# Kernel optimization log

Measured on AMD Instinct MI355X. Metric: run time of the kernel, lower is better.

The kernel has to match this reference:

```python
import jax, jax.numpy as jnp
import numpy as np

UPDATE_STEPS = 2
EPS = 1e-7


def _collect(attn, source, W, b):
    """_Collection_Unit: relu(Linear(source)) gathered by attention, row-averaged.
    attn: [N_tgt, N_src], source: [N_src, D_in], W: [D_out, D_in], b: [D_out]."""
    fc_out = jax.nn.relu(source @ W.T + b)          # [N_src, D_out]
    collect = attn @ fc_out                          # [N_tgt, D_out]
    denom = jnp.sum(attn, axis=1, keepdims=True) + EPS
    return collect / denom


def setup_inputs() -> dict:
    key = jax.random.key(0)
    ks = jax.random.split(key, 10)
    N_OBJ, N_REL, D = 2048, 16384, 1024
    inp = {
        "obj_feats": jax.random.normal(ks[0], (N_OBJ, D), jnp.float32),
        "rel_feats": jax.random.normal(ks[1], (N_REL, D), jnp.float32),
        "attn_sub": jax.random.uniform(ks[2], (N_OBJ, N_REL), jnp.float32),
        "attn_obj": jax.random.uniform(ks[3], (N_OBJ, N_REL), jnp.float32),
        "attn_self": jax.random.uniform(ks[4], (N_OBJ, N_OBJ), jnp.float32),
    }
    # normal_init(fc, 0, 0.01) per original module
    names = ["rel2obj_sub", "rel2obj_obj", "obj2rel_sub", "obj2rel_obj", "obj2obj"]
    for i, n in enumerate(names):
        inp[f"W_{n}"] = jax.random.normal(ks[5 + i], (D, D), jnp.float32) * 0.01
        inp[f"b_{n}"] = jnp.zeros((D,), jnp.float32)
    return inp


def reference(obj_feats, rel_feats, attn_sub, attn_obj, attn_self,
              W_rel2obj_sub, b_rel2obj_sub, W_rel2obj_obj, b_rel2obj_obj,
              W_obj2rel_sub, b_obj2rel_sub, W_obj2rel_obj, b_obj2rel_obj,
              W_obj2obj, b_obj2obj):
    x_obj, x_rel = obj_feats, rel_feats
    for _ in range(UPDATE_STEPS):
        # collect to objects: from relations (as subject / as object) and from other objects
        src_sub = _collect(attn_sub, x_rel, W_rel2obj_sub, b_rel2obj_sub)   # unit 0
        src_obj = _collect(attn_obj, x_rel, W_rel2obj_obj, b_rel2obj_obj)   # unit 1
        src_self = _collect(attn_self, x_obj, W_obj2obj, b_obj2obj)         # unit 4
        src2obj = (src_sub + src_obj + src_self) / 3.0
        x_obj_new = x_obj + src2obj                                          # _Update_Unit 0
        # collect to relations: from subject / object node features
        src_rel_sub = _collect(attn_sub.T, x_obj, W_obj2rel_sub, b_obj2rel_sub)  # unit 2
        src_rel_obj = _collect(attn_obj.T, x_obj, W_obj2rel_obj, b_obj2rel_obj)  # unit 3
        src2rel = (src_rel_sub + src_rel_obj) / 2.0
        x_rel = x_rel + src2rel                                              # _Update_Unit 1
        x_obj = x_obj_new
    return x_obj, x_rel
```

## Files before the change

kernel.cpp:

```cpp
#include <hip/hip_runtime.h>
#include <hip/hip_bf16.h>

typedef __attribute__((ext_vector_type(4))) float  f32x4;
typedef __attribute__((ext_vector_type(8))) __bf16 bf16x8;
typedef __attribute__((ext_vector_type(4))) int    i32x4;
typedef __attribute__((ext_vector_type(8))) int    i32x8;
typedef __hip_bfloat16 bf16_t;

#define GT 256
#define BM 128
#define BN 128
#define BK 32

#define NOBJ 2048
#define NREL 16384
#define DIM  1024
#define KOBJ 34816
#define KREL 4096

#define AS1Q __attribute__((address_space(1)))
#define AS3Q __attribute__((address_space(3)))

__device__ __forceinline__ void gload_lds16(const void* g, void* l) {
    __builtin_amdgcn_global_load_lds((AS1Q void*)const_cast<void*>(g),
                                     (AS3Q void*)l, 16, 0, 0);
}

#define MFMA_BF16 __builtin_amdgcn_mfma_f32_16x16x32_bf16
#define MFMA_F8(ACC, Af, Bf) \
    ACC = __builtin_amdgcn_mfma_scale_f32_16x16x128_f8f6f4( \
        Af, Bf, ACC, 0, 0, 0, 0x7F7F7F7F, 0, 0x7F7F7F7F)

__device__ __forceinline__ unsigned char fp8_byte(float x) {
    return (unsigned char)(__builtin_amdgcn_cvt_pk_fp8_f32(x, x, 0, false) & 0xFF);
}
__device__ __forceinline__ unsigned pk4_fp8(float a, float b, float c, float d) {
    int v = __builtin_amdgcn_cvt_pk_fp8_f32(a, b, 0, false);
    v = __builtin_amdgcn_cvt_pk_fp8_f32(c, d, v, true);
    return (unsigned)v;
}

__global__ __launch_bounds__(GT)
void gemm_bt_f234(const bf16_t* __restrict__ A, const bf16_t* __restrict__ B,
                  int M, int N, int K, const float* __restrict__ vecM,
                  unsigned char* __restrict__ fcRel8, unsigned char* __restrict__ fcObj8)
{
    __shared__ bf16_t sA[BM * BK];
    __shared__ bf16_t sB[BN * BK];

    const int tid  = threadIdx.x;
    const int lane = tid & 63;
    const int wid  = tid >> 6;
    const int wr = wid >> 1, wc = wid & 1;
    const int l15 = lane & 15, lk = lane >> 4;

    const long rowA0 = (long)blockIdx.x * BM;
    const long rowB0 = (long)blockIdx.y * BN;
    const long ldab  = (long)K * 2;

    const int c0 = tid, c1 = tid + GT;
    const int r0c = c0 >> 2, k0c = (c0 & 3) ^ ((r0c >> 1) & 3);
    const int r1c = c1 >> 2, k1c = (c1 & 3) ^ ((r1c >> 1) & 3);

    const char* gA0 = (const char*)A + (rowA0 + r0c) * ldab + k0c * 16;
    const char* gA1 = (const char*)A + (rowA0 + r1c) * ldab + k1c * 16;
    const char* gB0 = (const char*)B + (rowB0 + r0c) * ldab + k0c * 16;
    const char* gB1 = (const char*)B + (rowB0 + r1c) * ldab + k1c * 16;
    char* lA0 = (char*)sA + c0 * 16;
    char* lA1 = (char*)sA + c1 * 16;
    char* lB0 = (char*)sB + c0 * 16;
    char* lB1 = (char*)sB + c1 * 16;

    f32x4 acc[4][4];
    #pragma unroll
    for (int i = 0; i < 4; i++)
        #pragma unroll
        for (int j = 0; j < 4; j++) acc[i][j] = f32x4{0.f, 0.f, 0.f, 0.f};

    const int ktPer = K / BK;
    for (int kt = 0; kt < ktPer; ++kt) {
        const long kByte = (long)kt * (BK * 2);
        gload_lds16(gA0 + kByte, lA0);
        gload_lds16(gA1 + kByte, lA1);
        gload_lds16(gB0 + kByte, lB0);
        gload_lds16(gB1 + kByte, lB1);
        __syncthreads();

        bf16x8 af[4], bg[4];
        #pragma unroll
        for (int i = 0; i < 4; i++) {
            const int rr = wr * 64 + i * 16 + l15;
            const int kk = lk ^ ((rr >> 1) & 3);
            af[i] = *reinterpret_cast<const bf16x8*>((const char*)sA + rr * 64 + kk * 16);
        }
        #pragma unroll
        for (int j = 0; j < 4; j++) {
            const int rr = wc * 64 + j * 16 + l15;
            const int kk = lk ^ ((rr >> 1) & 3);
            bg[j] = *reinterpret_cast<const bf16x8*>((const char*)sB + rr * 64 + kk * 16);
        }
        #pragma unroll
        for (int i = 0; i < 4; i++)
            #pragma unroll
            for (int j = 0; j < 4; j++)
                acc[i][j] = MFMA_BF16(af[i], bg[j], acc[i][j], 0, 0, 0);
        __syncthreads();
    }

    #pragma unroll
    for (int i = 0; i < 4; i++) {
        const long mBase = rowA0 + wr * 64 + i * 16 + lk * 4;
        const f32x4 vm = *reinterpret_cast<const f32x4*>(&vecM[mBase]);
        #pragma unroll
        for (int r = 0; r < 4; r++) {
            const long m = mBase + r;
            #pragma unroll
            for (int j = 0; j < 4; j++) {
                const long n = rowB0 + wc * 64 + j * 16 + l15;
                const float v = fmaxf(acc[i][j][r] + vm[r], 0.f) * 64.f;
                const unsigned char o = fp8_byte(v);
                if (m < 1024)            fcRel8[m * (long)KREL + n] = o;
                else if (m < 2048)       fcRel8[(m - 1024) * (long)KREL + 2048 + n] = o;
                else                     fcObj8[(m - 2048) * (long)KOBJ + 32768 + n] = o;
            }
        }
    }
}

__global__ __launch_bounds__(512, 4)
void gemmf8fc(const unsigned char* __restrict__ A, const unsigned char* __restrict__ B,
              const float* __restrict__ bias, unsigned char* __restrict__ Cb8)
{
    __shared__ __align__(16) char lds[49152];

    const int tid  = threadIdx.x;
    const int lane = tid & 63;
    const int wid  = tid >> 6;
    const int wr = wid >> 2, wc = wid & 3;
    const int l15 = lane & 15, lk = lane >> 4;

    const int bid = blockIdx.x;
    const int s   = (bid & 7) * 128 + (bid >> 3);
    const long rowM0 = (long)(s >> 6) * 128;
    const long rowN0 = (long)(s & 63) * 256;
    const int  K  = 1024;
    const long ld = (long)K;
    const int  NT = K >> 7;

    const int rs = tid >> 3;
    const int kc = (tid & 7) ^ (rs & 7);
    const char* gA = (const char*)A + (rowM0 + rs) * ld + kc * 16;
    const char* gB = (const char*)B + (rowN0 + rs) * ld + kc * 16;
    char* lA = (char*)lds + tid * 16;
    char* lB = (char*)lds + 16384 + tid * 16;

    const int xc0 = ((2 * lk + 0) ^ (l15 & 7)) * 16;
    const int xc1 = ((2 * lk + 1) ^ (l15 & 7)) * 16;
    const int baseA = (wr * 64 + l15) * 128;
    const int baseB = 16384 + (wc * 64 + l15) * 128;

#define LDF8(dst, off) { \
    i32x4 lo_ = *(const i32x4*)((const char*)lds + (off) + xc0); \
    i32x4 hi_ = *(const i32x4*)((const char*)lds + (off) + xc1); \
    dst = __builtin_shufflevector(lo_, hi_, 0, 1, 2, 3, 4, 5, 6, 7); }

    f32x4 acc[4][4];
    #pragma unroll
    for (int i = 0; i < 4; i++)
        #pragma unroll
        for (int j = 0; j < 4; j++) acc[i][j] = f32x4{0.f, 0.f, 0.f, 0.f};

    for (int t = 0; t < NT; ++t) {
        const long kByte = (long)t * 128;
        gload_lds16(gA + kByte, lA);
        gload_lds16(gA + kByte + 64 * ld, lA + 8192);
        #pragma unroll
        for (int i = 0; i < 4; i++)
            gload_lds16(gB + kByte + (long)i * 64 * ld, lB + i * 8192);
        __syncthreads();

        i32x8 a[4];
        #pragma unroll
        for (int kf = 0; kf < 4; kf++) LDF8(a[kf], baseA + kf * 2048);
        #pragma unroll
        for (int j = 0; j < 4; j++) {
            i32x8 b;
            LDF8(b, baseB + j * 2048);
            #pragma unroll
            for (int kf = 0; kf < 4; kf++) MFMA_F8(acc[kf][j], a[kf], b);
        }
        __syncthreads();
    }
#undef LDF8

    #pragma unroll
    for (int kf = 0; kf < 4; kf++) {
        const long m0 = rowM0 + wr * 64 + kf * 16 + lk * 4;
        #pragma unroll
        for (int r = 0; r < 4; r++) {
            const long m = m0 + r;
            const float bs = 64.f * bias[m];
            #pragma unroll
            for (int j = 0; j < 4; j++) {
                const long n = rowN0 + wc * 64 + j * 16 + l15;
                const float v = fmaxf(acc[kf][j][r] + bs, 0.f);
                Cb8[(m & 1023) * (long)KOBJ + (m >> 10) * 16384 + n] = fp8_byte(v);
            }
        }
    }
}

__global__ __launch_bounds__(512, 4)
void gemmf8_dual(const unsigned char* __restrict__ Ao, const unsigned char* __restrict__ Bo,
                 float* __restrict__ Co,
                 const unsigned char* __restrict__ Ar, const unsigned char* __restrict__ Br,
                 float* __restrict__ Cr)
{
    __shared__ __align__(16) char lds[49152];

    const int tid  = threadIdx.x;
    const int lane = tid & 63;
    const int wid  = tid >> 6;
    const int wr = wid >> 2, wc = wid & 3;
    const int l15 = lane & 15, lk = lane >> 4;

    const int bid = blockIdx.x;
    const int s   = (bid & 7) * 128 + (bid >> 3);

    const unsigned char* A; const unsigned char* B; float* C;
    int K, NT; long kb0; float scale; bool at;
    long rowM0, rowN0;
    if (s < 512) {
        const int zz = s >> 6, t = s & 63;
        rowM0 = (long)(t >> 2) * 128; rowN0 = (long)(t & 3) * 256;
        A = Ao; B = Bo; C = Co;
        K = KOBJ; NT = 34; kb0 = (long)34 * zz * 128;
        scale = 1.f / (8192.f * 64.f); at = true;
    } else {
        const int t = s - 512;
        rowM0 = (long)(t >> 2) * 128; rowN0 = (long)(t & 3) * 256;
        A = Ar; B = Br; C = Cr;
        K = KREL; NT = 32; kb0 = 0;
        scale = 1.f / (2048.f * 64.f); at = false;
    }
    const long ld = (long)K;

    const int rs = tid >> 3;
    const int kc = (tid & 7) ^ (rs & 7);
    const char* gA = (const char*)A + (rowM0 + rs) * ld + kb0 + kc * 16;
    const char* gB = (const char*)B + (rowN0 + rs) * ld + kb0 + kc * 16;
    char* lA = (char*)lds + tid * 16;
    char* lB = (char*)lds + 16384 + tid * 16;

    const int xc0 = ((2 * lk + 0) ^ (l15 & 7)) * 16;
    const int xc1 = ((2 * lk + 1) ^ (l15 & 7)) * 16;
    const int baseA = (wr * 64 + l15) * 128;
    const int baseB = 16384 + (wc * 64 + l15) * 128;

#define LDF8(dst, off) { \
    i32x4 lo_ = *(const i32x4*)((const char*)lds + (off) + xc0); \
    i32x4 hi_ = *(const i32x4*)((const char*)lds + (off) + xc1); \
    dst = __builtin_shufflevector(lo_, hi_, 0, 1, 2, 3, 4, 5, 6, 7); }

    f32x4 acc[4][4];
    #pragma unroll
    for (int i = 0; i < 4; i++)
        #pragma unroll
        for (int j = 0; j < 4; j++) acc[i][j] = f32x4{0.f, 0.f, 0.f, 0.f};

    for (int t = 0; t < NT; ++t) {
        const long kByte = (long)t * 128;
        gload_lds16(gA + kByte, lA);
        gload_lds16(gA + kByte + 64 * ld, lA + 8192);
        #pragma unroll
        for (int i = 0; i < 4; i++)
            gload_lds16(gB + kByte + (long)i * 64 * ld, lB + i * 8192);
        __syncthreads();

        i32x8 a[4];
        #pragma unroll
        for (int kf = 0; kf < 4; kf++) LDF8(a[kf], baseA + kf * 2048);
        #pragma unroll
        for (int j = 0; j < 4; j++) {
            i32x8 b;
            LDF8(b, baseB + j * 2048);
            #pragma unroll
            for (int kf = 0; kf < 4; kf++) MFMA_F8(acc[kf][j], a[kf], b);
        }
        __syncthreads();
    }
#undef LDF8

    #pragma unroll
    for (int kf = 0; kf < 4; kf++) {
        const long m0 = rowM0 + wr * 64 + kf * 16 + lk * 4;
        #pragma unroll
        for (int r = 0; r < 4; r++) {
            const long m = m0 + r;
            #pragma unroll
            for (int j = 0; j < 4; j++) {
                const long n = rowN0 + wc * 64 + j * 16 + l15;
                const float v = acc[kf][j][r] * scale;
                if (at) atomicAdd(&C[m * (long)DIM + n], v);
                else    C[m * (long)DIM + n] += v;
            }
        }
    }
}

__global__ __launch_bounds__(256)
void k_cast_bf16(const float* __restrict__ in, bf16_t* __restrict__ out, long n)
{
    const long stride = (long)gridDim.x * blockDim.x;
    for (long i = (long)blockIdx.x * blockDim.x + threadIdx.x; i * 4 < n; i += stride) {
        f32x4 v = *reinterpret_cast<const f32x4*>(in + i * 4);
        union { bf16_t h[4]; ushort4 u; } o;
        o.h[0] = __float2bfloat16(v[0]); o.h[1] = __float2bfloat16(v[1]);
        o.h[2] = __float2bfloat16(v[2]); o.h[3] = __float2bfloat16(v[3]);
        *reinterpret_cast<ushort4*>(out + i * 4) = o.u;
    }
}

__global__ __launch_bounds__(256)
void k_cast_fp8(const float* __restrict__ in, unsigned char* __restrict__ out,
                long n, float scale)
{
    const long stride = (long)gridDim.x * blockDim.x;
    for (long i = (long)blockIdx.x * blockDim.x + threadIdx.x; i * 4 < n; i += stride) {
        f32x4 v = *reinterpret_cast<const f32x4*>(in + i * 4);
        *reinterpret_cast<unsigned*>(out + i * 4) =
            pk4_fp8(v[0] * scale, v[1] * scale, v[2] * scale, v[3] * scale);
    }
}

template<bool COLS>
__global__ __launch_bounds__(256)
void k_sums(const float* __restrict__ in, int C,
            float* __restrict__ rowsum, float* __restrict__ colsum)
{
    __shared__ float cpart[16][64];
    __shared__ float rpart[64][17];
    const int tid = threadIdx.x;
    const int tx  = tid & 15;
    const int ty  = tid >> 4;
    const long c0 = (long)blockIdx.x * 64;
    const long r0 = (long)blockIdx.y * 64;

    float cs0 = 0.f, cs1 = 0.f, cs2 = 0.f, cs3 = 0.f;
    #pragma unroll
    for (int i = 0; i < 4; i++) {
        const int r = i * 16 + ty;
        const f32x4 v = *reinterpret_cast<const f32x4*>(&in[(r0 + r) * (long)C + c0 + tx * 4]);
        rpart[r][tx] = v[0] + v[1] + v[2] + v[3];
        cs0 += v[0]; cs1 += v[1]; cs2 += v[2]; cs3 += v[3];
    }
    if (COLS) {
        cpart[ty][tx * 4 + 0] = cs0;
        cpart[ty][tx * 4 + 1] = cs1;
        cpart[ty][tx * 4 + 2] = cs2;
        cpart[ty][tx * 4 + 3] = cs3;
    }
    __syncthreads();
    if (tid < 64) {
        float rs = 0.f;
        #pragma unroll
        for (int k = 0; k < 16; k++) rs += rpart[tid][k];
        atomicAdd(&rowsum[r0 + tid], rs);
        if (COLS) {
            float cs = 0.f;
            #pragma unroll
            for (int k = 0; k < 16; k++) cs += cpart[k][tid];
            atomicAdd(&colsum[c0 + tid], cs);
        }
    }
}

__global__ __launch_bounds__(256)
void k_invscale(float* __restrict__ s, int n, float c)
{
    const int i = blockIdx.x * 256 + threadIdx.x;
    if (i < n) s[i] = c / (s[i] + 1e-7f);
}

template<bool TRANS>
__global__ __launch_bounds__(256)
void k_prep2f8(const float* __restrict__ in, int C,
               unsigned char* __restrict__ Aobj, unsigned char* __restrict__ Arel,
               const float* __restrict__ invRow, const float* __restrict__ invCol)
{
    __shared__ float tile[64][65];
    const int tid = threadIdx.x;
    const int tx  = tid & 15;
    const int ty  = tid >> 4;
    const long c0 = (long)blockIdx.x * 64;
    const long r0 = (long)blockIdx.y * 64;

    #pragma unroll
    for (int i = 0; i < 4; i++) {
        const int r = i * 16 + ty;
        const f32x4 v = *reinterpret_cast<const f32x4*>(&in[(r0 + r) * (long)C + c0 + tx * 4]);
        const float sc = invRow[r0 + r];
        *reinterpret_cast<unsigned*>(&Aobj[(r0 + r) * (long)KOBJ + c0 + tx * 4]) =
            pk4_fp8(v[0] * sc, v[1] * sc, v[2] * sc, v[3] * sc);
        if (TRANS) *reinterpret_cast<f32x4*>(&tile[r][tx * 4]) = v;
    }
    if (TRANS) {
        __syncthreads();
        const int rr = tid & 63;
        const int cg = tid >> 6;
        #pragma unroll
        for (int i = 0; i < 16; i++) {
            const int c = cg * 16 + i;
            const float sc = invCol[c0 + c];
            Arel[(c0 + c) * (long)KREL + r0 + rr] = fp8_byte(tile[rr][c] * sc);
        }
    }
}

extern "C" void kernel_launch(void* const* d_in, const int* in_sizes, int n_in,
                              void* d_out, int out_size, void* d_ws, size_t ws_size,
                              hipStream_t stream)
{
    if (n_in < 15) return;
    const float* obj_feats = (const float*)d_in[0];
    const float* rel_feats = (const float*)d_in[1];
    const float* attn_sub  = (const float*)d_in[2];
    const float* attn_obj  = (const float*)d_in[3];
    const float* attn_self = (const float*)d_in[4];
    const float* Wf[5] = { (const float*)d_in[5], (const float*)d_in[7],
                           (const float*)d_in[9], (const float*)d_in[11], (const float*)d_in[13] };
    const float* Bf[5] = { (const float*)d_in[6], (const float*)d_in[8],
                           (const float*)d_in[10], (const float*)d_in[12], (const float*)d_in[14] };

    const int NO = NOBJ, NR = NREL, D = DIM;

    char* w = (char*)d_ws;
    auto take = [&](size_t bytes) { char* p = w; w += bytes; return p; };
    unsigned char* Aobj8  = (unsigned char*)take((size_t)NO * KOBJ);
    unsigned char* Arel8  = (unsigned char*)take((size_t)NR * KREL);
    unsigned char* fcObj8 = (unsigned char*)take((size_t)D * KOBJ);
    unsigned char* fcRel8 = (unsigned char*)take((size_t)D * KREL);
    unsigned char* xrel8  = (unsigned char*)take((size_t)NR * D);
    unsigned char* W018   = (unsigned char*)take((size_t)2 * D * D);
    bf16_t* xobj_bf = (bf16_t*)take((size_t)NO * D * 2);
    bf16_t* Wstk234 = (bf16_t*)take((size_t)3 * D * D * 2);
    float*  b01     = (float*)take((size_t)2 * D * 4);
    float*  bstk    = (float*)take((size_t)3 * D * 4);
    float*  sums    = (float*)take((size_t)(3 * NO + 2 * NR) * 4);
    float* invS     = sums;
    float* invO     = sums + NO;
    float* invSelf  = sums + 2 * NO;
    float* invTS    = sums + 3 * NO;
    float* invTO    = sums + 3 * NO + NR;
    if ((size_t)(w - (char*)d_ws) > ws_size) return;

    float* x_obj = (float*)d_out;
    float* x_rel = x_obj + (size_t)NO * D;

    hipMemcpyAsync(x_obj, obj_feats, (size_t)NO * D * 4, hipMemcpyDeviceToDevice, stream);
    hipMemcpyAsync(x_rel, rel_feats, (size_t)NR * D * 4, hipMemcpyDeviceToDevice, stream);
    hipMemcpyAsync(b01,     Bf[0], (size_t)D * 4, hipMemcpyDeviceToDevice, stream);
    hipMemcpyAsync(b01 + D, Bf[1], (size_t)D * 4, hipMemcpyDeviceToDevice, stream);
    for (int i = 0; i < 3; i++)
        hipMemcpyAsync(bstk + i * D, Bf[2 + i], (size_t)D * 4, hipMemcpyDeviceToDevice, stream);
    hipMemsetAsync(sums, 0, (size_t)(3 * NO + 2 * NR) * 4, stream);

    auto castb = [&](const float* in, bf16_t* out, long n) {
        long blocks = (n / 4 + 255) / 256; if (blocks > 4096) blocks = 4096;
        k_cast_bf16<<<dim3((unsigned)blocks), dim3(256), 0, stream>>>(in, out, n);
    };
    auto cast8 = [&](const float* in, unsigned char* out, long n, float sc) {
        long blocks = (n / 4 + 255) / 256; if (blocks > 4096) blocks = 4096;
        k_cast_fp8<<<dim3((unsigned)blocks), dim3(256), 0, stream>>>(in, out, n, sc);
    };
    cast8(Wf[0], W018,                 (long)D * D, 64.f);
    cast8(Wf[1], W018 + (size_t)D * D, (long)D * D, 64.f);
    for (int i = 0; i < 3; i++)
        castb(Wf[2 + i], Wstk234 + (size_t)i * D * D, (long)D * D);

    k_sums<true><<<dim3(NR / 64, NO / 64), dim3(256), 0, stream>>>(attn_sub, NR, invS, invTS);
    k_sums<true><<<dim3(NR / 64, NO / 64), dim3(256), 0, stream>>>(attn_obj, NR, invO, invTO);
    k_sums<false><<<dim3(NO / 64, NO / 64), dim3(256), 0, stream>>>(attn_self, NO, invSelf, nullptr);
    k_invscale<<<dim3((3 * NO + 255) / 256), dim3(256), 0, stream>>>(sums, 3 * NO, 8192.f / 3.f);
    k_invscale<<<dim3((2 * NR + 255) / 256), dim3(256), 0, stream>>>(sums + 3 * NO, 2 * NR, 1024.f);

    k_prep2f8<true><<<dim3(NR / 64, NO / 64), dim3(256), 0, stream>>>(
        attn_sub, NR, Aobj8, Arel8, invS, invTS);
    k_prep2f8<true><<<dim3(NR / 64, NO / 64), dim3(256), 0, stream>>>(
        attn_obj, NR, Aobj8 + 16384, Arel8 + 2048, invO, invTO);
    k_prep2f8<false><<<dim3(NO / 64, NO / 64), dim3(256), 0, stream>>>(
        attn_self, NO, Aobj8 + 32768, nullptr, invSelf, nullptr);

    for (int step = 0; step < 2; ++step) {
        castb(x_obj, xobj_bf, (long)NO * D);
        cast8(x_rel, xrel8, (long)NR * D, 1.f);

        gemmf8fc<<<dim3(1024), dim3(512), 0, stream>>>(W018, xrel8, b01, fcObj8);
        gemm_bt_f234<<<dim3(3 * D / BM, NO / BN, 1), dim3(GT), 0, stream>>>(
            Wstk234, xobj_bf, 3 * D, NO, D, bstk, fcRel8, fcObj8);

        gemmf8_dual<<<dim3(1024), dim3(512), 0, stream>>>(
            Aobj8, fcObj8, x_obj, Arel8, fcRel8, x_rel);
    }
}
```

Measured before the change: 813.8 us.

## Merge object-side FC GEMMs into FP8 MLP kernel and fuse x_rel FP8 cast into update

Replaces the bf16 GEMM for units 2-4 with FP8 by casting those weights and x_obj to FP8. That GEMM is merged with the relation-side FC GEMM into one launch of 1216 blocks, and a block-index branch picks the operands. The relation update epilogue now also writes the FP8 copy of x_rel, so the separate per-step x_rel cast pass goes away. This cuts kernel launches, memory traffic and matrix-core cost, but lowers the precision of the object-feature MLP to FP8.

```diff
diff --git a/kernel.cpp b/kernel.cpp
--- a/kernel.cpp
+++ b/kernel.cpp
@@ -7,11 +7,6 @@
 typedef __attribute__((ext_vector_type(8))) int    i32x8;
 typedef __hip_bfloat16 bf16_t;
 
-#define GT 256
-#define BM 128
-#define BN 128
-#define BK 32
-
 #define NOBJ 2048
 #define NREL 16384
 #define DIM  1024
@@ -26,7 +21,6 @@
                                      (AS3Q void*)l, 16, 0, 0);
 }
 
-#define MFMA_BF16 __builtin_amdgcn_mfma_f32_16x16x32_bf16
 #define MFMA_F8(ACC, Af, Bf) \
     ACC = __builtin_amdgcn_mfma_scale_f32_16x16x128_f8f6f4( \
         Af, Bf, ACC, 0, 0, 0, 0x7F7F7F7F, 0, 0x7F7F7F7F)
@@ -40,96 +34,11 @@
     return (unsigned)v;
 }
 
-__global__ __launch_bounds__(GT)
-void gemm_bt_f234(const bf16_t* __restrict__ A, const bf16_t* __restrict__ B,
-                  int M, int N, int K, const float* __restrict__ vecM,
-                  unsigned char* __restrict__ fcRel8, unsigned char* __restrict__ fcObj8)
-{
-    __shared__ bf16_t sA[BM * BK];
-    __shared__ bf16_t sB[BN * BK];
-
-    const int tid  = threadIdx.x;
-    const int lane = tid & 63;
-    const int wid  = tid >> 6;
-    const int wr = wid >> 1, wc = wid & 1;
-    const int l15 = lane & 15, lk = lane >> 4;
-
-    const long rowA0 = (long)blockIdx.x * BM;
-    const long rowB0 = (long)blockIdx.y * BN;
-    const long ldab  = (long)K * 2;
-
-    const int c0 = tid, c1 = tid + GT;
-    const int r0c = c0 >> 2, k0c = (c0 & 3) ^ ((r0c >> 1) & 3);
-    const int r1c = c1 >> 2, k1c = (c1 & 3) ^ ((r1c >> 1) & 3);
-
-    const char* gA0 = (const char*)A + (rowA0 + r0c) * ldab + k0c * 16;
-    const char* gA1 = (const char*)A + (rowA0 + r1c) * ldab + k1c * 16;
-    const char* gB0 = (const char*)B + (rowB0 + r0c) * ldab + k0c * 16;
-    const char* gB1 = (const char*)B + (rowB0 + r1c) * ldab + k1c * 16;
-    char* lA0 = (char*)sA + c0 * 16;
-    char* lA1 = (char*)sA + c1 * 16;
-    char* lB0 = (char*)sB + c0 * 16;
-    char* lB1 = (char*)sB + c1 * 16;
-
-    f32x4 acc[4][4];
-    #pragma unroll
-    for (int i = 0; i < 4; i++)
-        #pragma unroll
-        for (int j = 0; j < 4; j++) acc[i][j] = f32x4{0.f, 0.f, 0.f, 0.f};
-
-    const int ktPer = K / BK;
-    for (int kt = 0; kt < ktPer; ++kt) {
-        const long kByte = (long)kt * (BK * 2);
-        gload_lds16(gA0 + kByte, lA0);
-        gload_lds16(gA1 + kByte, lA1);
-        gload_lds16(gB0 + kByte, lB0);
-        gload_lds16(gB1 + kByte, lB1);
-        __syncthreads();
-
-        bf16x8 af[4], bg[4];
-        #pragma unroll
-        for (int i = 0; i < 4; i++) {
-            const int rr = wr * 64 + i * 16 + l15;
-            const int kk = lk ^ ((rr >> 1) & 3);
-            af[i] = *reinterpret_cast<const bf16x8*>((const char*)sA + rr * 64 + kk * 16);
-        }
-        #pragma unroll
-        for (int j = 0; j < 4; j++) {
-            const int rr = wc * 64 + j * 16 + l15;
-            const int kk = lk ^ ((rr >> 1) & 3);
-            bg[j] = *reinterpret_cast<const bf16x8*>((const char*)sB + rr * 64 + kk * 16);
-        }
-        #pragma unroll
-        for (int i = 0; i < 4; i++)
-            #pragma unroll
-            for (int j = 0; j < 4; j++)
-                acc[i][j] = MFMA_BF16(af[i], bg[j], acc[i][j], 0, 0, 0);
-        __syncthreads();
-    }
-
-    #pragma unroll
-    for (int i = 0; i < 4; i++) {
-        const long mBase = rowA0 + wr * 64 + i * 16 + lk * 4;
-        const f32x4 vm = *reinterpret_cast<const f32x4*>(&vecM[mBase]);
-        #pragma unroll
-        for (int r = 0; r < 4; r++) {
-            const long m = mBase + r;
-            #pragma unroll
-            for (int j = 0; j < 4; j++) {
-                const long n = rowB0 + wc * 64 + j * 16 + l15;
-                const float v = fmaxf(acc[i][j][r] + vm[r], 0.f) * 64.f;
-                const unsigned char o = fp8_byte(v);
-                if (m < 1024)            fcRel8[m * (long)KREL + n] = o;
-                else if (m < 2048)       fcRel8[(m - 1024) * (long)KREL + 2048 + n] = o;
-                else                     fcObj8[(m - 2048) * (long)KOBJ + 32768 + n] = o;
-            }
-        }
-    }
-}
-
 __global__ __launch_bounds__(512, 4)
-void gemmf8fc(const unsigned char* __restrict__ A, const unsigned char* __restrict__ B,
-              const float* __restrict__ bias, unsigned char* __restrict__ Cb8)
+void gemmf8mlp(const unsigned char* __restrict__ W01, const unsigned char* __restrict__ xrel8,
+               const unsigned char* __restrict__ W234, const unsigned char* __restrict__ xobj8,
+               const float* __restrict__ b01, const float* __restrict__ bstk,
+               unsigned char* __restrict__ fcObj8, unsigned char* __restrict__ fcRel8)
 {
     __shared__ __align__(16) char lds[49152];
 
@@ -140,12 +49,22 @@
     const int l15 = lane & 15, lk = lane >> 4;
 
     const int bid = blockIdx.x;
-    const int s   = (bid & 7) * 128 + (bid >> 3);
-    const long rowM0 = (long)(s >> 6) * 128;
-    const long rowN0 = (long)(s & 63) * 256;
-    const int  K  = 1024;
-    const long ld = (long)K;
-    const int  NT = K >> 7;
+    const int s   = (bid & 7) * 152 + (bid >> 3);
+
+    const unsigned char* A; const unsigned char* B; const float* bias; bool isFC;
+    long rowM0, rowN0;
+    if (s < 1024) {
+        rowM0 = (long)(s >> 6) * 128;
+        rowN0 = (long)(s & 63) * 256;
+        A = W01; B = xrel8; bias = b01; isFC = true;
+    } else {
+        const int t = s - 1024;
+        rowM0 = (long)(t >> 3) * 128;
+        rowN0 = (long)(t & 7) * 256;
+        A = W234; B = xobj8; bias = bstk; isFC = false;
+    }
+    const long ld = DIM;
+    const int  NT = DIM >> 7;
 
     const int rs = tid >> 3;
     const int kc = (tid & 7) ^ (rs & 7);
@@ -204,7 +123,14 @@
             for (int j = 0; j < 4; j++) {
                 const long n = rowN0 + wc * 64 + j * 16 + l15;
                 const float v = fmaxf(acc[kf][j][r] + bs, 0.f);
-                Cb8[(m & 1023) * (long)KOBJ + (m >> 10) * 16384 + n] = fp8_byte(v);
+                const unsigned char o = fp8_byte(v);
+                if (isFC) {
+                    fcObj8[(m & 1023) * (long)KOBJ + (m >> 10) * 16384 + n] = o;
+                } else {
+                    if (m < 1024)       fcRel8[m * (long)KREL + n] = o;
+                    else if (m < 2048)  fcRel8[(m - 1024) * (long)KREL + 2048 + n] = o;
+                    else                fcObj8[(m - 2048) * (long)KOBJ + 32768 + n] = o;
+                }
             }
         }
     }
@@ -214,7 +140,7 @@
 void gemmf8_dual(const unsigned char* __restrict__ Ao, const unsigned char* __restrict__ Bo,
                  float* __restrict__ Co,
                  const unsigned char* __restrict__ Ar, const unsigned char* __restrict__ Br,
-                 float* __restrict__ Cr)
+                 float* __restrict__ Cr, unsigned char* __restrict__ xrel8out)
 {
     __shared__ __align__(16) char lds[49152];
 
@@ -301,23 +227,16 @@
             for (int j = 0; j < 4; j++) {
                 const long n = rowN0 + wc * 64 + j * 16 + l15;
                 const float v = acc[kf][j][r] * scale;
-                if (at) atomicAdd(&C[m * (long)DIM + n], v);
-                else    C[m * (long)DIM + n] += v;
+                const long idx = m * (long)DIM + n;
+                if (at) {
+                    atomicAdd(&C[idx], v);
+                } else {
+                    const float nv = C[idx] + v;
+                    C[idx] = nv;
+                    xrel8out[idx] = fp8_byte(nv);
+                }
             }
         }
-    }
-}
-
-__global__ __launch_bounds__(256)
-void k_cast_bf16(const float* __restrict__ in, bf16_t* __restrict__ out, long n)
-{
-    const long stride = (long)gridDim.x * blockDim.x;
-    for (long i = (long)blockIdx.x * blockDim.x + threadIdx.x; i * 4 < n; i += stride) {
-        f32x4 v = *reinterpret_cast<const f32x4*>(in + i * 4);
-        union { bf16_t h[4]; ushort4 u; } o;
-        o.h[0] = __float2bfloat16(v[0]); o.h[1] = __float2bfloat16(v[1]);
-        o.h[2] = __float2bfloat16(v[2]); o.h[3] = __float2bfloat16(v[3]);
-        *reinterpret_cast<ushort4*>(out + i * 4) = o.u;
     }
 }
 
@@ -441,9 +360,9 @@
     unsigned char* fcObj8 = (unsigned char*)take((size_t)D * KOBJ);
     unsigned char* fcRel8 = (unsigned char*)take((size_t)D * KREL);
     unsigned char* xrel8  = (unsigned char*)take((size_t)NR * D);
+    unsigned char* xobj8  = (unsigned char*)take((size_t)NO * D);
     unsigned char* W018   = (unsigned char*)take((size_t)2 * D * D);
-    bf16_t* xobj_bf = (bf16_t*)take((size_t)NO * D * 2);
-    bf16_t* Wstk234 = (bf16_t*)take((size_t)3 * D * D * 2);
+    unsigned char* W2348  = (unsigned char*)take((size_t)3 * D * D);
     float*  b01     = (float*)take((size_t)2 * D * 4);
     float*  bstk    = (float*)take((size_t)3 * D * 4);
     float*  sums    = (float*)take((size_t)(3 * NO + 2 * NR) * 4);
@@ -465,10 +384,6 @@
         hipMemcpyAsync(bstk + i * D, Bf[2 + i], (size_t)D * 4, hipMemcpyDeviceToDevice, stream);
     hipMemsetAsync(sums, 0, (size_t)(3 * NO + 2 * NR) * 4, stream);
 
-    auto castb = [&](const float* in, bf16_t* out, long n) {
-        long blocks = (n / 4 + 255) / 256; if (blocks > 4096) blocks = 4096;
-        k_cast_bf16<<<dim3((unsigned)blocks), dim3(256), 0, stream>>>(in, out, n);
-    };
     auto cast8 = [&](const float* in, unsigned char* out, long n, float sc) {
         long blocks = (n / 4 + 255) / 256; if (blocks > 4096) blocks = 4096;
         k_cast_fp8<<<dim3((unsigned)blocks), dim3(256), 0, stream>>>(in, out, n, sc);
@@ -476,7 +391,7 @@
     cast8(Wf[0], W018,                 (long)D * D, 64.f);
     cast8(Wf[1], W018 + (size_t)D * D, (long)D * D, 64.f);
     for (int i = 0; i < 3; i++)
-        castb(Wf[2 + i], Wstk234 + (size_t)i * D * D, (long)D * D);
+        cast8(Wf[2 + i], W2348 + (size_t)i * D * D, (long)D * D, 64.f);
 
     k_sums<true><<<dim3(NR / 64, NO / 64), dim3(256), 0, stream>>>(attn_sub, NR, invS, invTS);
     k_sums<true><<<dim3(NR / 64, NO / 64), dim3(256), 0, stream>>>(attn_obj, NR, invO, invTO);
@@ -491,15 +406,15 @@
     k_prep2f8<false><<<dim3(NO / 64, NO / 64), dim3(256), 0, stream>>>(
         attn_self, NO, Aobj8 + 32768, nullptr, invSelf, nullptr);
 
+    cast8(x_rel, xrel8, (long)NR * D, 1.f);
+
     for (int step = 0; step < 2; ++step) {
-        castb(x_obj, xobj_bf, (long)NO * D);
-        cast8(x_rel, xrel8, (long)NR * D, 1.f);
-
-        gemmf8fc<<<dim3(1024), dim3(512), 0, stream>>>(W018, xrel8, b01, fcObj8);
-        gemm_bt_f234<<<dim3(3 * D / BM, NO / BN, 1), dim3(GT), 0, stream>>>(
-            Wstk234, xobj_bf, 3 * D, NO, D, bstk, fcRel8, fcObj8);
+        cast8(x_obj, xobj8, (long)NO * D, 1.f);
+
+        gemmf8mlp<<<dim3(1216), dim3(512), 0, stream>>>(
+            W018, xrel8, W2348, xobj8, b01, bstk, fcObj8, fcRel8);
 
         gemmf8_dual<<<dim3(1024), dim3(512), 0, stream>>>(
-            Aobj8, fcObj8, x_obj, Arel8, fcRel8, x_rel);
-    }
-}
+            Aobj8, fcObj8, x_obj, Arel8, fcRel8, x_rel, xrel8);
+    }
+}
```

New measurement: 772.0 us. 5.1% less time.
